# Optimization experiments

Hardware: AMD Instinct MI355X
Metric: run time of the kernel (lower is better)

## Reference

```python
import jax, jax.numpy as jnp
import numpy as np

C = 128
GROUPS = 8
EPS = 1e-5


def setup_inputs() -> dict:
    key = jax.random.key(0)
    ks = jax.random.split(key, 7)
    B, D, H, W = 2, 8, 32, 32
    x = jax.random.normal(ks[0], (B, C, D, H, W), dtype=jnp.float32)
    gamma = jnp.ones((C,), dtype=jnp.float32)
    beta = jnp.zeros((C,), dtype=jnp.float32)
    w_qkv = jax.random.normal(ks[1], (3 * C, C), dtype=jnp.float32) * 0.02
    b_qkv = jnp.zeros((3 * C,), dtype=jnp.float32)
    w_proj = jax.random.normal(ks[2], (C, C), dtype=jnp.float32) * 0.02
    b_proj = jnp.zeros((C,), dtype=jnp.float32)
    return {"x": x, "gamma": gamma, "beta": beta, "w_qkv": w_qkv,
            "b_qkv": b_qkv, "w_proj": w_proj, "b_proj": b_proj}


def _group_norm(x, gamma, beta):
    B, Cc, D, H, W = x.shape
    xg = x.reshape(B, GROUPS, Cc // GROUPS, D, H, W)
    mean = jnp.mean(xg, axis=(2, 3, 4, 5), keepdims=True)
    var = jnp.var(xg, axis=(2, 3, 4, 5), keepdims=True)
    xn = (xg - mean) * jax.lax.rsqrt(var + EPS)
    xn = xn.reshape(B, Cc, D, H, W)
    return xn * gamma[None, :, None, None, None] + beta[None, :, None, None, None]


def reference(x, gamma, beta, w_qkv, b_qkv, w_proj, b_proj):
    B, Cc, D, H, W = x.shape
    N = D * H * W
    h = _group_norm(x, gamma, beta)
    # 1x1x1 conv == per-voxel matmul over channels
    qkv = jnp.einsum('bcdhw,oc->bodhw', h, w_qkv) + b_qkv[None, :, None, None, None]
    q, k, v = jnp.split(qkv, 3, axis=1)  # each [B, C, D, H, W]
    q = q.reshape(B, Cc, N).transpose(0, 2, 1)  # [B, N, C]
    k = k.reshape(B, Cc, N).transpose(0, 2, 1)
    v = v.reshape(B, Cc, N).transpose(0, 2, 1)
    scale = Cc ** (-0.5)
    attn = jax.nn.softmax(jnp.einsum('bnc,bmc->bnm', q, k) * scale, axis=-1)
    h = jnp.einsum('bnm,bmc->bnc', attn, v)  # [B, N, C]
    h = h.transpose(0, 2, 1).reshape(B, Cc, D, H, W)
    out = jnp.einsum('bcdhw,oc->bodhw', h, w_proj) + b_proj[None, :, None, None, None]
    return x + out
```

## Files before the change

### kernel.cpp

```cpp
#include <hip/hip_runtime.h>

typedef __bf16 bf16x8 __attribute__((ext_vector_type(8)));
typedef float  f32x4  __attribute__((ext_vector_type(4)));
typedef float  f32x16 __attribute__((ext_vector_type(16)));
typedef float  f32x2  __attribute__((ext_vector_type(2)));
typedef unsigned int uint32;
typedef unsigned int u32x2 __attribute__((ext_vector_type(2)));
typedef unsigned int u32x4 __attribute__((ext_vector_type(4)));
typedef int i32x4 __attribute__((ext_vector_type(4)));
typedef int i32x8 __attribute__((ext_vector_type(8)));
typedef long long i64;
typedef long long i64x4v __attribute__((ext_vector_type(4)));

#define MFMA16(a, b, c) __builtin_amdgcn_mfma_f32_16x16x32_bf16((a), (b), (c), 0, 0, 0)
#define MFMA32F8(a, b, c) __builtin_amdgcn_mfma_f32_32x32x16_fp8_fp8((a), (b), (c), 0, 0, 0)
#define GLL(gsrc, ldst) __builtin_amdgcn_global_load_lds( \
    (const __attribute__((address_space(1))) uint32*)(gsrc), \
    (__attribute__((address_space(3))) uint32*)(ldst), 16, 0, 0)

static constexpr int Cch = 128;
static constexpr int Nvox = 8192;

__device__ inline f32x16 mx4(i32x8 a, i32x8 b, f32x16 c) {
#if __has_builtin(__builtin_amdgcn_mfma_scale_f32_32x32x64_f8f6f4)
  return __builtin_amdgcn_mfma_scale_f32_32x32x64_f8f6f4(
      a, b, c, 0 , 0 ,
      0, 0x7F7F7F7Fu, 0, 0x7F7F7F7Fu );
#else
  i64x4v av = __builtin_bit_cast(i64x4v, a);
  i64x4v bv = __builtin_bit_cast(i64x4v, b);
  c = MFMA32F8(av[0], bv[0], c);
  c = MFMA32F8(av[1], bv[1], c);
  c = MFMA32F8(av[2], bv[2], c);
  c = MFMA32F8(av[3], bv[3], c);
  return c;
#endif
}

__device__ inline unsigned int pkbf(float x, float y) {
  unsigned short ux = __builtin_bit_cast(unsigned short, (__bf16)x);
  unsigned short uy = __builtin_bit_cast(unsigned short, (__bf16)y);
  return (unsigned int)ux | ((unsigned int)uy << 16);
}

__device__ inline unsigned int pk4fp8(float a, float b, float c, float d) {
  int w = 0;
  w = __builtin_amdgcn_cvt_pk_fp8_f32(a, b, w, false);
  w = __builtin_amdgcn_cvt_pk_fp8_f32(c, d, w, true);
  return (unsigned int)w;
}
__device__ inline unsigned char fp8b(float x) {
  return (unsigned char)(__builtin_amdgcn_cvt_pk_fp8_f32(x, x, 0, false) & 0xff);
}

__device__ inline void lane32_swap(unsigned int& x, unsigned int& y) {
#if __has_builtin(__builtin_amdgcn_permlane32_swap)
  auto r = __builtin_amdgcn_permlane32_swap(x, y, false, false);
  x = r[0]; y = r[1];
#else
  unsigned int sx = (unsigned int)__shfl_xor((int)x, 32);
  unsigned int sy = (unsigned int)__shfl_xor((int)y, 32);
  bool lo = ((threadIdx.x & 63) < 32);
  unsigned int nx = lo ? x : sy;
  unsigned int ny = lo ? sx : y;
  x = nx; y = ny;
#endif
}
__device__ inline float red32_sum(float v) {
  unsigned int a = __builtin_bit_cast(unsigned int, v), b = a;
  lane32_swap(a, b);
  return __builtin_bit_cast(float, a) + __builtin_bit_cast(float, b);
}

__global__ __launch_bounds__(256) void gn_part_k(const float* __restrict__ x,
                                                 f32x2* __restrict__ part,
                                                 const float* __restrict__ wq,
                                                 const float* __restrict__ wp,
                                                 __bf16* __restrict__ wqb,
                                                 __bf16* __restrict__ wpb) {
  int wi = blockIdx.x * 256 + threadIdx.x;
  if (wi < 49152) wqb[wi] = (__bf16)wq[wi];
  else wpb[wi - 49152] = (__bf16)wp[wi - 49152];

  int bg = blockIdx.x >> 4, pt = blockIdx.x & 15;
  const f32x4* xb = (const f32x4*)(x + (size_t)bg * 131072 + (size_t)pt * 8192);
  float s = 0.f, ss = 0.f;
  for (int i = threadIdx.x; i < 2048; i += 256) {
    f32x4 v = xb[i];
    s += (v.x + v.y) + (v.z + v.w);
    ss += (v.x * v.x + v.y * v.y) + (v.z * v.z + v.w * v.w);
  }
#pragma unroll
  for (int off = 32; off; off >>= 1) {
    s  += __shfl_down(s, off);
    ss += __shfl_down(ss, off);
  }
  __shared__ float rb[4], rbss[4];
  if ((threadIdx.x & 63) == 0) { rb[threadIdx.x >> 6] = s; rbss[threadIdx.x >> 6] = ss; }
  __syncthreads();
  if (threadIdx.x == 0) {
    f32x2 o; o.x = rb[0] + rb[1] + rb[2] + rb[3];
    o.y = rbss[0] + rbss[1] + rbss[2] + rbss[3];
    part[blockIdx.x] = o;
  }
}

__global__ __launch_bounds__(256) void gn_apply_k(const float* __restrict__ x,
                                                  const float* __restrict__ gamma,
                                                  const float* __restrict__ beta,
                                                  const f32x2* __restrict__ part,
                                                  __bf16* __restrict__ xn) {
  __shared__ __bf16 t[64][136];
  __shared__ float sm_mean[16], sm_rstd[16];
  int tid = threadIdx.x;
  {
    f32x2 v = part[tid];
    float s = v.x, ss = v.y;
#pragma unroll
    for (int off = 1; off < 16; off <<= 1) {
      s += __shfl_xor(s, off);
      ss += __shfl_xor(ss, off);
    }
    if ((tid & 15) == 0) {
      int bg = tid >> 4;
      const float invn = 1.f / 131072.f;
      float mean = s * invn;
      float var = ss * invn - mean * mean;
      sm_mean[bg] = mean;
      sm_rstd[bg] = rsqrtf(var + 1e-5f);
    }
  }
  __syncthreads();
  int b = blockIdx.x >> 7;
  int n0 = (blockIdx.x & 127) << 6;
  const float* xb = x + (size_t)b * Cch * Nvox;
  for (int i = threadIdx.x; i < 128 * 64; i += 256) {
    int c = i >> 6, nl = i & 63;
    int g = c >> 4;
    float mean = sm_mean[b * 8 + g];
    float rstd = sm_rstd[b * 8 + g];
    float v = xb[(size_t)c * Nvox + n0 + nl];
    t[nl][c] = (__bf16)((v - mean) * rstd * gamma[c] + beta[c]);
  }
  __syncthreads();
  __bf16* outb = xn + (size_t)b * Nvox * Cch;
  for (int i = threadIdx.x; i < 64 * 16; i += 256) {
    int row = i >> 4, ch = (i & 15) << 3;
    *reinterpret_cast<bf16x8*>(&outb[(size_t)(n0 + row) * Cch + ch]) =
        *reinterpret_cast<const bf16x8*>(&t[row][ch]);
  }
}

__global__ __launch_bounds__(256) void qkv_k(const __bf16* __restrict__ xn,
                                             const __bf16* __restrict__ wq,
                                             const float* __restrict__ b_qkv,
                                             unsigned char* __restrict__ q8,
                                             unsigned char* __restrict__ k8,
                                             unsigned char* __restrict__ v8t) {
  __shared__ __bf16 xt[64][136];
  __shared__ unsigned char vtl[64][64];
  int id = blockIdx.x;
  int b = id >> 7;
  int n0 = (id & 127) * 64;
  int w = threadIdx.x >> 6, l = threadIdx.x & 63;
  int lr = l & 15, lh = l >> 4;
  const float k2 = 0.08838834764831845f * 1.4426950408889634f;

  const __bf16* xb = xn + ((size_t)b * Nvox + n0) * Cch;
  for (int i = threadIdx.x; i < 64 * 16; i += 256) {
    int row = i >> 4, ch = (i & 15) << 3;
    *reinterpret_cast<bf16x8*>(&xt[row][ch]) =
        *reinterpret_cast<const bf16x8*>(&xb[(size_t)row * Cch + ch]);
  }
  __syncthreads();

#pragma unroll
  for (int ot = 0; ot < 6; ++ot) {
    int o0b = ot * 64;
    int ow = o0b + w * 16;
    bf16x8 a[4];
#pragma unroll
    for (int kc = 0; kc < 4; kc++)
      a[kc] = *reinterpret_cast<const bf16x8*>(
          &wq[(size_t)(ow + lr) * 128 + kc * 32 + lh * 8]);

#pragma unroll
    for (int ns = 0; ns < 4; ns++) {
      f32x4 acc = {0.f, 0.f, 0.f, 0.f};
#pragma unroll
      for (int kc = 0; kc < 4; kc++) {
        bf16x8 bf = *reinterpret_cast<const bf16x8*>(
            &xt[ns * 16 + lr][kc * 32 + lh * 8]);
        acc = MFMA16(a[kc], bf, acc);
      }
      int o0 = ow + lh * 4;
      int n = n0 + ns * 16 + lr;
      float f0 = acc[0] + b_qkv[o0 + 0];
      float f1 = acc[1] + b_qkv[o0 + 1];
      float f2 = acc[2] + b_qkv[o0 + 2];
      float f3 = acc[3] + b_qkv[o0 + 3];
      if (ot < 2) {
        *reinterpret_cast<unsigned int*>(
            q8 + ((size_t)b * Nvox + n) * 128 + o0) =
            pk4fp8(f0 * k2, f1 * k2, f2 * k2, f3 * k2);
      } else if (ot < 4) {
        *reinterpret_cast<unsigned int*>(
            k8 + ((size_t)b * Nvox + n) * 128 + (o0 - 128)) =
            pk4fp8(f0, f1, f2, f3);
      } else {
        int crel = w * 16 + lh * 4;
        int kk = ns * 16 + lr;
        int r4 = kk & 15;
        int hh = (r4 >> 2) & 1;
        int jj = (r4 & 3) + (((r4 >> 3) & 1) << 2);
        int m = ((kk >> 5) << 5) + (hh << 4) + (((kk >> 4) & 1) << 3) + jj;
        vtl[crel + 0][m] = fp8b(f0);
        vtl[crel + 1][m] = fp8b(f1);
        vtl[crel + 2][m] = fp8b(f2);
        vtl[crel + 3][m] = fp8b(f3);
      }
    }
    if (ot >= 4) {
      __syncthreads();
      int cbase = (ot - 4) * 64;
      int row = threadIdx.x >> 2, seg = threadIdx.x & 3;
      *reinterpret_cast<u32x4*>(
          v8t + ((size_t)b * Cch + cbase + row) * Nvox + n0 + seg * 16) =
          *reinterpret_cast<const u32x4*>(&vtl[row][seg * 16]);
      __syncthreads();
    }
  }
}

__global__ __launch_bounds__(256, 2) void attn_k(const unsigned char* __restrict__ q,
                                                 const unsigned char* __restrict__ kk,
                                                 const unsigned char* __restrict__ vt,
                                                 __bf16* __restrict__ po0,
                                                 __bf16* __restrict__ po1,
                                                 __bf16* __restrict__ po2,
                                                 __bf16* __restrict__ po3,
                                                 f32x2* __restrict__ ml) {
  extern __shared__ char smem[];
  const int bi = blockIdx.x;
  const int kq = bi & 3;
  const int b = (bi >> 2) & 1;
  const int qgrp = bi >> 3;
  const int w = threadIdx.x >> 6;
  const int l = threadIdx.x & 63;
  const int l31 = l & 31, h = l >> 5;
  const int swl16 = (l31 & 15) << 4;

  const char* kbase = (const char*)kk + ((size_t)b * 8192 + (size_t)kq * 2048) * 128;
  const char* vbase = (const char*)vt + (size_t)b * 1048576 + (size_t)kq * 2048;

  const unsigned char* qrow = q +
      ((size_t)b * 8192 + (size_t)qgrp * 128 + (size_t)w * 32 + l31) * 128 + h * 32;
  i32x8 qa8[2];
#pragma unroll
  for (int dc = 0; dc < 2; dc++) {
    i32x4 q0 = *reinterpret_cast<const i32x4*>(qrow + dc * 64);
    i32x4 q1 = *reinterpret_cast<const i32x4*>(qrow + dc * 64 + 16);
    qa8[dc] = __builtin_shufflevector(q0, q1, 0, 1, 2, 3, 4, 5, 6, 7);
  }

  f32x16 O[4];
#pragma unroll
  for (int cb = 0; cb < 4; cb++)
#pragma unroll
    for (int r = 0; r < 16; r++) O[cb][r] = 0.f;
  float s0 = 0.f, s1 = 0.f, s2 = 0.f, s3 = 0.f;

  auto stage = [&](int t, int bs) {
    if (w < 2) {
      const char* kt = kbase + (size_t)t * 64 * 128;
      char* dst = smem + bs * 16384;
#pragma unroll
      for (int it = 0; it < 4; ++it) {
        int ob = (w * 4 + it) * 1024;
        int o = ob + l * 16;
        int row = o >> 8;
        int lcol = (o & 255) ^ ((row & 15) << 4);
        int ksel = lcol >> 7, c = lcol & 127;
        GLL(kt + (size_t)(ksel * 32 + row) * 128 + c, dst + ob);
      }
    } else {
      const char* vtile = vbase + (size_t)t * 64;
      char* dst = smem + bs * 16384 + 8192;
#pragma unroll
      for (int it = 0; it < 4; ++it) {
        int ob = ((w - 2) * 4 + it) * 1024;
        int o = ob + l * 16;
        int row = o >> 8;
        int lcol = (o & 255) ^ ((row & 15) << 4);
        int cs = lcol >> 6, k16 = lcol & 63;
        GLL(vtile + (size_t)(cs * 32 + row) * 8192 + k16, dst + ob);
      }
    }
  };

  stage(0, 0);
  int cur = 0;
  const int NT = 32;

  for (int t = 0; t < NT; ++t) {
    asm volatile("s_waitcnt vmcnt(0) lgkmcnt(0)" ::: "memory");
    __builtin_amdgcn_sched_barrier(0);
    __syncthreads();
    if (t + 1 < NT) stage(t + 1, cur ^ 1);

    const char* Kb = smem + cur * 16384;
    const char* Vb = Kb + 8192;

    f32x16 St[2];
#pragma unroll
    for (int ks = 0; ks < 2; ks++)
#pragma unroll
      for (int r = 0; r < 16; r++) St[ks][r] = 0.f;
    __builtin_amdgcn_s_setprio(1);
#pragma unroll
    for (int ks = 0; ks < 2; ks++) {
#pragma unroll
      for (int dc = 0; dc < 2; dc++) {
        int base = ks * 128 + dc * 64 + h * 32;
        i32x4 k0 = *reinterpret_cast<const i32x4*>(
            Kb + (size_t)l31 * 256 + (base ^ swl16));
        i32x4 k1 = *reinterpret_cast<const i32x4*>(
            Kb + (size_t)l31 * 256 + ((base + 16) ^ swl16));
        St[ks] = mx4(__builtin_shufflevector(k0, k1, 0, 1, 2, 3, 4, 5, 6, 7),
                     qa8[dc], St[ks]);
      }
    }
    __builtin_amdgcn_s_setprio(0);

#pragma unroll
    for (int ks = 0; ks < 2; ks++)
#pragma unroll
      for (int r = 0; r < 16; r++)
        St[ks][r] = __builtin_amdgcn_exp2f(St[ks][r]);
#pragma unroll
    for (int ks = 0; ks < 2; ks++)
#pragma unroll
      for (int r = 0; r < 16; r += 4) {
        s0 += St[ks][r + 0]; s1 += St[ks][r + 1];
        s2 += St[ks][r + 2]; s3 += St[ks][r + 3];
      }

    i32x8 pb;
#pragma unroll
    for (int ks = 0; ks < 2; ks++) {
      pb[ks * 4 + 0] = (int)pk4fp8(St[ks][0],  St[ks][1],  St[ks][2],  St[ks][3]);
      pb[ks * 4 + 1] = (int)pk4fp8(St[ks][4],  St[ks][5],  St[ks][6],  St[ks][7]);
      pb[ks * 4 + 2] = (int)pk4fp8(St[ks][8],  St[ks][9],  St[ks][10], St[ks][11]);
      pb[ks * 4 + 3] = (int)pk4fp8(St[ks][12], St[ks][13], St[ks][14], St[ks][15]);
    }

    __builtin_amdgcn_s_setprio(1);
#pragma unroll
    for (int cb = 0; cb < 4; cb++) {
      int vb0 = cb * 64 + h * 16;
      i32x4 v0 = *reinterpret_cast<const i32x4*>(
          Vb + (size_t)l31 * 256 + (vb0 ^ swl16));
      i32x4 v1 = *reinterpret_cast<const i32x4*>(
          Vb + (size_t)l31 * 256 + ((vb0 + 32) ^ swl16));
      O[cb] = mx4(__builtin_shufflevector(v0, v1, 0, 1, 2, 3, 4, 5, 6, 7),
                  pb, O[cb]);
    }
    __builtin_amdgcn_s_setprio(0);
    cur ^= 1;
  }

  float lsum = red32_sum((s0 + s1) + (s2 + s3));
  __bf16* po = (kq == 0) ? po0 : (kq == 1) ? po1 : (kq == 2) ? po2 : po3;
  int qg = b * 8192 + qgrp * 128 + w * 32 + l31;
#pragma unroll
  for (int cb = 0; cb < 4; cb++) {
#pragma unroll
    for (int rq = 0; rq < 4; rq++) {
      int c = cb * 32 + rq * 8 + h * 4;
      u32x2 wv;
      wv[0] = pkbf(O[cb][rq * 4 + 0], O[cb][rq * 4 + 1]);
      wv[1] = pkbf(O[cb][rq * 4 + 2], O[cb][rq * 4 + 3]);
      *reinterpret_cast<u32x2*>((char*)po + ((size_t)qg * 128 + c) * 2) = wv;
    }
  }
  if (l < 32) {
    f32x2 v; v.x = 0.f; v.y = lsum;
    ml[(size_t)kq * 16384 + qg] = v;
  }
}

__global__ __launch_bounds__(256) void proj_k(const __bf16* __restrict__ po0,
                                              const __bf16* __restrict__ po1,
                                              const __bf16* __restrict__ po2,
                                              const __bf16* __restrict__ po3,
                                              const f32x2* __restrict__ ml,
                                              const __bf16* __restrict__ wp,
                                              const float* __restrict__ b_proj,
                                              const float* __restrict__ x,
                                              float* __restrict__ out) {
  int id = blockIdx.x;
  int b = id >> 8;
  int co0 = ((id >> 7) & 1) * 64;
  int n0 = (id & 127) * 64;
  int w = threadIdx.x >> 6, l = threadIdx.x & 63;
  int lr = l & 15, lh = l >> 4;
  int cow = co0 + w * 16;

  bf16x8 a[4];
#pragma unroll
  for (int kc = 0; kc < 4; kc++)
    a[kc] = *reinterpret_cast<const bf16x8*>(&wp[(size_t)(cow + lr) * 128 + kc * 32 + lh * 8]);

#pragma unroll
  for (int ns = 0; ns < 4; ns++) {
    int n = n0 + ns * 16 + lr;
    int qg = b * 8192 + n;
    f32x2 a0 = ml[qg], a1 = ml[16384 + qg], a2 = ml[32768 + qg], a3 = ml[49152 + qg];
    float M = fmaxf(fmaxf(a0.x, a1.x), fmaxf(a2.x, a3.x));
    float e0 = __builtin_amdgcn_exp2f(a0.x - M);
    float e1 = __builtin_amdgcn_exp2f(a1.x - M);
    float e2 = __builtin_amdgcn_exp2f(a2.x - M);
    float e3 = __builtin_amdgcn_exp2f(a3.x - M);
    float invL = 1.f / (e0 * a0.y + e1 * a1.y + e2 * a2.y + e3 * a3.y);
    float c0f = e0 * invL, c1f = e1 * invL, c2f = e2 * invL, c3f = e3 * invL;

    f32x4 acc = {0.f, 0.f, 0.f, 0.f};
#pragma unroll
    for (int kc = 0; kc < 4; kc++) {
      size_t off = (size_t)qg * 128 + kc * 32 + lh * 8;
      bf16x8 v0 = *reinterpret_cast<const bf16x8*>(&po0[off]);
      bf16x8 v1 = *reinterpret_cast<const bf16x8*>(&po1[off]);
      bf16x8 v2 = *reinterpret_cast<const bf16x8*>(&po2[off]);
      bf16x8 v3 = *reinterpret_cast<const bf16x8*>(&po3[off]);
      bf16x8 hv;
#pragma unroll
      for (int i = 0; i < 8; i++)
        hv[i] = (__bf16)(c0f * (float)v0[i] + c1f * (float)v1[i] +
                         c2f * (float)v2[i] + c3f * (float)v3[i]);
      acc = MFMA16(a[kc], hv, acc);
    }
#pragma unroll
    for (int r2 = 0; r2 < 4; r2++) {
      int co = cow + lh * 4 + r2;
      size_t idx = ((size_t)b * Cch + co) * Nvox + n;
      out[idx] = x[idx] + b_proj[co] + acc[r2];
    }
  }
}

extern "C" void kernel_launch(void* const* d_in, const int* in_sizes, int n_in,
                              void* d_out, int out_size, void* d_ws, size_t ws_size,
                              hipStream_t stream) {
  const float* x      = (const float*)d_in[0];
  const float* gamma  = (const float*)d_in[1];
  const float* beta   = (const float*)d_in[2];
  const float* w_qkv  = (const float*)d_in[3];
  const float* b_qkv  = (const float*)d_in[4];
  const float* w_proj = (const float*)d_in[5];
  const float* b_proj = (const float*)d_in[6];
  float* out = (float*)d_out;

  char* ws = (char*)d_ws;
  f32x2*  part  = (f32x2*)(ws + 256);
  __bf16* wq_b  = (__bf16*)(ws + 4096);
  __bf16* wp_b  = (__bf16*)(ws + 4096 + 98304);
  size_t base = 135168;
  const size_t SZ = (size_t)2 * Nvox * Cch * sizeof(__bf16);
  __bf16* xn  = (__bf16*)(ws + base + 0 * SZ);
  unsigned char* q8  = (unsigned char*)(ws + base + 1 * SZ);
  unsigned char* k8  = (unsigned char*)(ws + base + 2 * SZ);
  unsigned char* v8t = (unsigned char*)(ws + base + 3 * SZ);
  __bf16* hw  = (__bf16*)(ws + base + 4 * SZ);
  f32x2*  ml  = (f32x2*)(ws + base + 5 * SZ);
  __bf16* po2 = (__bf16*)(ws + base + 5 * SZ + 524288);
  __bf16* po3 = (__bf16*)(ws + base + 5 * SZ + 524288 + SZ);

  (void)hipFuncSetAttribute((const void*)attn_k,
                            hipFuncAttributeMaxDynamicSharedMemorySize, 32768);

  gn_part_k<<<256, 256, 0, stream>>>(x, part, w_qkv, w_proj, wq_b, wp_b);
  gn_apply_k<<<256, 256, 0, stream>>>(x, gamma, beta, part, xn);
  qkv_k<<<256, 256, 0, stream>>>(xn, wq_b, b_qkv, q8, k8, v8t);
  attn_k<<<512, 256, 32768, stream>>>(q8, k8, v8t, hw, xn, po2, po3, ml);
  proj_k<<<512, 256, 0, stream>>>(hw, xn, po2, po3, ml, wp_b, b_proj, x, out);
}
```

Before: 86.00 us.

## Software-pipeline attention loop so PV of previous tile overlaps QK of current

The attention inner loop now issues the P·V MFMAs for the previous key tile right after the current tile's Q·K MFMAs, and defers the last tile's P·V to an epilogue. A third LDS buffer keeps the previous V tile alive, which raises dynamic shared memory from 32 KB to 48 KB per block. The intent is to hide the exp/fp8-pack latency between the two matmuls behind independent MFMA work. In exchange it uses more LDS and keeps the packed probabilities live across iterations, which may reduce occupancy.

```diff
diff --git a/kernel.cpp b/kernel.cpp
--- a/kernel.cpp
+++ b/kernel.cpp
@@ -269,6 +269,7 @@
 #pragma unroll
     for (int r = 0; r < 16; r++) O[cb][r] = 0.f;
   float s0 = 0.f, s1 = 0.f, s2 = 0.f, s3 = 0.f;
+  i32x8 pbp = {};
 
   auto stage = [&](int t, int bs) {
     if (w < 2) {
@@ -299,17 +300,17 @@
   };
 
   stage(0, 0);
-  int cur = 0;
+  int prv = 2, cur = 0, nxt = 1;
   const int NT = 32;
 
   for (int t = 0; t < NT; ++t) {
     asm volatile("s_waitcnt vmcnt(0) lgkmcnt(0)" ::: "memory");
     __builtin_amdgcn_sched_barrier(0);
     __syncthreads();
-    if (t + 1 < NT) stage(t + 1, cur ^ 1);
+    if (t + 1 < NT) stage(t + 1, nxt);
 
     const char* Kb = smem + cur * 16384;
-    const char* Vb = Kb + 8192;
+    const char* Vbp = smem + prv * 16384 + 8192;
 
     f32x16 St[2];
 #pragma unroll
@@ -330,6 +331,18 @@
                      qa8[dc], St[ks]);
       }
     }
+    if (t > 0) {
+#pragma unroll
+      for (int cb = 0; cb < 4; cb++) {
+        int vb0 = cb * 64 + h * 16;
+        i32x4 v0 = *reinterpret_cast<const i32x4*>(
+            Vbp + (size_t)l31 * 256 + (vb0 ^ swl16));
+        i32x4 v1 = *reinterpret_cast<const i32x4*>(
+            Vbp + (size_t)l31 * 256 + ((vb0 + 32) ^ swl16));
+        O[cb] = mx4(__builtin_shufflevector(v0, v1, 0, 1, 2, 3, 4, 5, 6, 7),
+                    pbp, O[cb]);
+      }
+    }
     __builtin_amdgcn_s_setprio(0);
 
 #pragma unroll
@@ -344,29 +357,31 @@
         s0 += St[ks][r + 0]; s1 += St[ks][r + 1];
         s2 += St[ks][r + 2]; s3 += St[ks][r + 3];
       }
-
-    i32x8 pb;
 #pragma unroll
     for (int ks = 0; ks < 2; ks++) {
-      pb[ks * 4 + 0] = (int)pk4fp8(St[ks][0],  St[ks][1],  St[ks][2],  St[ks][3]);
-      pb[ks * 4 + 1] = (int)pk4fp8(St[ks][4],  St[ks][5],  St[ks][6],  St[ks][7]);
-      pb[ks * 4 + 2] = (int)pk4fp8(St[ks][8],  St[ks][9],  St[ks][10], St[ks][11]);
-      pb[ks * 4 + 3] = (int)pk4fp8(St[ks][12], St[ks][13], St[ks][14], St[ks][15]);
-    }
-
+      pbp[ks * 4 + 0] = (int)pk4fp8(St[ks][0],  St[ks][1],  St[ks][2],  St[ks][3]);
+      pbp[ks * 4 + 1] = (int)pk4fp8(St[ks][4],  St[ks][5],  St[ks][6],  St[ks][7]);
+      pbp[ks * 4 + 2] = (int)pk4fp8(St[ks][8],  St[ks][9],  St[ks][10], St[ks][11]);
+      pbp[ks * 4 + 3] = (int)pk4fp8(St[ks][12], St[ks][13], St[ks][14], St[ks][15]);
+    }
+
+    int op = prv; prv = cur; cur = nxt; nxt = op;
+  }
+
+  {
+    const char* Vbp = smem + prv * 16384 + 8192;
     __builtin_amdgcn_s_setprio(1);
 #pragma unroll
     for (int cb = 0; cb < 4; cb++) {
       int vb0 = cb * 64 + h * 16;
       i32x4 v0 = *reinterpret_cast<const i32x4*>(
-          Vb + (size_t)l31 * 256 + (vb0 ^ swl16));
+          Vbp + (size_t)l31 * 256 + (vb0 ^ swl16));
       i32x4 v1 = *reinterpret_cast<const i32x4*>(
-          Vb + (size_t)l31 * 256 + ((vb0 + 32) ^ swl16));
+          Vbp + (size_t)l31 * 256 + ((vb0 + 32) ^ swl16));
       O[cb] = mx4(__builtin_shufflevector(v0, v1, 0, 1, 2, 3, 4, 5, 6, 7),
-                  pb, O[cb]);
+                  pbp, O[cb]);
     }
     __builtin_amdgcn_s_setprio(0);
-    cur ^= 1;
   }
 
   float lsum = red32_sum((s0 + s1) + (s2 + s3));
@@ -476,11 +491,11 @@
   __bf16* po3 = (__bf16*)(ws + base + 5 * SZ + 524288 + SZ);
 
   (void)hipFuncSetAttribute((const void*)attn_k,
-                            hipFuncAttributeMaxDynamicSharedMemorySize, 32768);
+                            hipFuncAttributeMaxDynamicSharedMemorySize, 49152);
 
   gn_part_k<<<256, 256, 0, stream>>>(x, part, w_qkv, w_proj, wq_b, wp_b);
   gn_apply_k<<<256, 256, 0, stream>>>(x, gamma, beta, part, xn);
   qkv_k<<<256, 256, 0, stream>>>(xn, wq_b, b_qkv, q8, k8, v8t);
-  attn_k<<<512, 256, 32768, stream>>>(q8, k8, v8t, hw, xn, po2, po3, ml);
+  attn_k<<<512, 256, 49152, stream>>>(q8, k8, v8t, hw, xn, po2, po3, ml);
   proj_k<<<512, 256, 0, stream>>>(hw, xn, po2, po3, ml, wp_b, b_proj, x, out);
 }
```

Measured after the change: 86.29 us. Within noise of the previous version (+0.3%).
